# Performance work log

Measured on AMD Instinct MI355X. Metric: run time of the kernel, lower is better.

The kernel has to match this reference:

```python
import jax, jax.numpy as jnp
import numpy as np

B, T_NEW, D_MODEL, H, DH = 8, 512, 1024, 16, 64
CACHED = 2048
T_TOTAL = CACHED + T_NEW  # static padded total length (last batch item is full)


def setup_inputs() -> dict:
    key = jax.random.key(0)
    ks = jax.random.split(key, 16)
    x_new = jax.random.normal(ks[0], (B, T_NEW, D_MODEL), jnp.float32)
    past_lengths = jax.random.randint(ks[1], (B,), CACHED // 2, CACHED)
    past_lengths = past_lengths.at[-1].set(CACHED).astype(jnp.int32)
    new_counts = jax.random.randint(ks[2], (B,), 1, T_NEW)
    new_counts = new_counts.at[-1].set(T_NEW).astype(jnp.int32)
    # prefix (left-aligned) valid mask for new tokens, matching how the torch
    # module compacts k_new[b, :, :count] into the cache
    valid_new_mask = jnp.arange(T_NEW)[None, :] < new_counts[:, None]
    total_lengths = past_lengths + new_counts
    key_padding_mask = jnp.arange(T_TOTAL)[None, :] < total_lengths[:, None]
    inv_freq = 1.0 / (10000.0 ** (jnp.arange(0, DH, 2, dtype=jnp.float32) / DH))
    pm = (jnp.arange(CACHED)[None, :] < past_lengths[:, None])[:, None, :, None]
    past_k = jax.random.normal(ks[3], (B, H, CACHED, DH), jnp.float32) * pm
    past_v = jax.random.normal(ks[4], (B, H, CACHED, DH), jnp.float32) * pm
    s = 0.02
    Wq = jax.random.normal(ks[5], (D_MODEL, D_MODEL), jnp.float32) * s
    Wk = jax.random.normal(ks[6], (D_MODEL, D_MODEL), jnp.float32) * s
    Wv = jax.random.normal(ks[7], (D_MODEL, D_MODEL), jnp.float32) * s
    Wo = jax.random.normal(ks[8], (D_MODEL, D_MODEL), jnp.float32) * s
    bq = jnp.zeros((D_MODEL,), jnp.float32)
    bk = jnp.zeros((D_MODEL,), jnp.float32)
    bv = jnp.zeros((D_MODEL,), jnp.float32)
    bo = jnp.zeros((D_MODEL,), jnp.float32)
    return {
        'x_new': x_new, 'inv_freq': inv_freq, 'past_k': past_k, 'past_v': past_v,
        'Wq': Wq, 'bq': bq, 'Wk': Wk, 'bk': bk, 'Wv': Wv, 'bv': bv, 'Wo': Wo, 'bo': bo,
        'key_padding_mask': key_padding_mask, 'past_lengths': past_lengths,
        'valid_new_mask': valid_new_mask,
    }


def _rotate_half(x):
    h = x.shape[-1] // 2
    return jnp.concatenate([-x[..., h:], x[..., :h]], axis=-1)


def reference(x_new, inv_freq, past_k, past_v, Wq, bq, Wk, bk, Wv, bv, Wo, bo,
              key_padding_mask, past_lengths, valid_new_mask):
    Bb, Tn, _ = x_new.shape
    # projections -> [B, H, T_new, DH]
    q = (x_new @ Wq.T + bq).reshape(Bb, Tn, H, DH).transpose(0, 2, 1, 3)
    k_new = (x_new @ Wk.T + bk).reshape(Bb, Tn, H, DH).transpose(0, 2, 1, 3)
    v_new = (x_new @ Wv.T + bv).reshape(Bb, Tn, H, DH).transpose(0, 2, 1, 3)
    # RoPE at absolute positions past_len + step (invalid -> 0)
    steps = jnp.arange(Tn)
    positions = jnp.where(valid_new_mask, past_lengths[:, None] + steps[None, :], 0)
    freqs = positions[..., None].astype(jnp.float32) * inv_freq  # [B, T, DH/2]
    emb = jnp.concatenate([freqs, freqs], axis=-1)
    cos = jnp.cos(emb)[:, None].astype(q.dtype)  # [B, 1, T, DH]
    sin = jnp.sin(emb)[:, None].astype(q.dtype)
    q = q * cos + _rotate_half(q) * sin
    k_new = k_new * cos + _rotate_half(k_new) * sin
    vm = valid_new_mask[:, None, :, None].astype(q.dtype)
    q = q * vm
    k_new = k_new * vm
    v_new = v_new * vm
    # zero cached entries past each item's cached length (matches padded cache)
    pm = (jnp.arange(CACHED)[None, :] < past_lengths[:, None])[:, None, :, None]
    past_k = past_k * pm.astype(past_k.dtype)
    past_v = past_v * pm.astype(past_v.dtype)
    # ragged append: scatter new tokens at [past_len, past_len+count); invalid
    # tokens dumped into an extra slot T_TOTAL that is sliced off
    pos_idx = jnp.where(valid_new_mask, past_lengths[:, None] + steps[None, :], T_TOTAL)
    pad = lambda p: jnp.pad(p, ((0, 0), (0, 0), (0, T_TOTAL + 1 - CACHED), (0, 0)))
    scat = jax.vmap(lambda base, new, idx: base.at[:, idx, :].add(new))
    k_total = scat(pad(past_k), k_new, pos_idx)[:, :, :T_TOTAL]
    v_total = scat(pad(past_v), v_new, pos_idx)[:, :, :T_TOTAL]
    # padded SDPA with key-padding mask
    scores = jnp.einsum('bhqd,bhkd->bhqk', q, k_total) / jnp.sqrt(jnp.asarray(DH, q.dtype))
    scores = jnp.where(key_padding_mask[:, None, None, :], scores, jnp.finfo(scores.dtype).min)
    attn = jax.nn.softmax(scores, axis=-1)
    ctx = jnp.einsum('bhqk,bhkd->bhqd', attn, v_total)
    ctx = ctx.transpose(0, 2, 1, 3).reshape(Bb, Tn, D_MODEL)
    out = (ctx @ Wo.T + bo) * valid_new_mask[..., None].astype(ctx.dtype)
    total_lengths = past_lengths + valid_new_mask.sum(axis=1).astype(past_lengths.dtype)
    return out, k_total, v_total, total_lengths
```

## Files before the change

### kernel.cpp

```cpp
#include <hip/hip_runtime.h>
#include <math.h>

#define B_ 8
#define TN 512
#define DM 1024
#define H_ 16
#define DH 64
#define CACHED_ 2048
#define TT 2560

#define QSC 0.18033688011112042f

typedef __attribute__((ext_vector_type(8))) short bf16x8;
typedef __attribute__((ext_vector_type(4))) float f32x4;

union U16x8 { uint4 u; unsigned short s[8]; };
union U16x4 { uint2 u; unsigned short s[4]; };
union F4 { float4 v; float f[4]; };

__device__ __forceinline__ unsigned short f2b(float x) {
    unsigned u = __float_as_uint(x);
    unsigned r = (u + 0x7FFFu + ((u >> 16) & 1u)) >> 16;
    return (unsigned short)r;
}
__device__ __forceinline__ float b2f(unsigned short v) {
    return __uint_as_float((unsigned)v << 16);
}

__device__ __forceinline__ void gload16(const void* g, void* l) {
    __builtin_amdgcn_global_load_lds(
        (const __attribute__((address_space(1))) void*)g,
        (__attribute__((address_space(3))) void*)l, 16, 0, 0);
}

__global__ void count_kernel(const unsigned char* __restrict__ vnm,
                             const unsigned char* __restrict__ kpm,
                             const int* __restrict__ past_len,
                             int* __restrict__ counts,
                             float* __restrict__ total_out) {
    int b = blockIdx.x;
    __shared__ int red[256];
    int esz = (kpm[1] | kpm[2] | kpm[3]) ? 1 : 4;
    int s = 0;
    for (int t = threadIdx.x; t < TN; t += 256)
        s += (vnm[(size_t)(b * TN + t) * esz] != 0) ? 1 : 0;
    red[threadIdx.x] = s;
    __syncthreads();
    for (int off = 128; off > 0; off >>= 1) {
        if (threadIdx.x < off) red[threadIdx.x] += red[threadIdx.x + off];
        __syncthreads();
    }
    if (threadIdx.x == 0) {
        counts[b] = red[0];
        total_out[b] = (float)(past_len[b] + red[0]);
    }
}

__global__ void cvt_all(const float* __restrict__ x,
                        const float* __restrict__ Wq,
                        const float* __restrict__ Wk,
                        const float* __restrict__ Wv,
                        const float* __restrict__ Wo,
                        unsigned short* __restrict__ Xbf,
                        unsigned short* __restrict__ Wqkvb,
                        unsigned short* __restrict__ Wob) {
    int i8 = (blockIdx.x * 256 + threadIdx.x) << 3;
    const float* src;
    unsigned short* dst;
    int off;
    if (i8 < (1 << 22)) {
        src = x; off = i8; dst = Xbf + i8;
    } else if (i8 < (1 << 22) + (3 << 20)) {
        int j = i8 - (1 << 22);
        int w = j >> 20;
        src = w == 0 ? Wq : (w == 1 ? Wk : Wv);
        off = j & 0xFFFFF;
        dst = Wqkvb + j;
    } else {
        int j = i8 - ((1 << 22) + (3 << 20));
        src = Wo; off = j; dst = Wob + j;
    }
    float4 a = *(const float4*)(src + off);
    float4 b = *(const float4*)(src + off + 4);
    U16x8 o;
    o.s[0] = f2b(a.x); o.s[1] = f2b(a.y); o.s[2] = f2b(a.z); o.s[3] = f2b(a.w);
    o.s[4] = f2b(b.x); o.s[5] = f2b(b.y); o.s[6] = f2b(b.z); o.s[7] = f2b(b.w);
    *(uint4*)dst = o.u;
}

__device__ __forceinline__ void gemm_core(
    const unsigned short* __restrict__ A, const unsigned short* __restrict__ Bw,
    int K, int m0, int n0, short* As, short* Bs, f32x4 acc[4][4]) {
    const int tid = threadIdx.x;
    const int wave = tid >> 6, lane = tid & 63;
    const int wm = wave >> 1, wn = wave & 1;
    const int l15 = lane & 15, lq = lane >> 4;

    const int srow = wave * 16 + (lane >> 2);
    const int sc = (lane & 3) << 3;
    const unsigned short* Ag0 = A + (size_t)(m0 + srow) * K + sc;
    const unsigned short* Ag1 = A + (size_t)(m0 + 64 + srow) * K + sc;
    const unsigned short* Bg0 = Bw + (size_t)(n0 + srow) * K + sc;
    const unsigned short* Bg1 = Bw + (size_t)(n0 + 64 + srow) * K + sc;
    short* Ad0 = As + wave * 16 * 32;
    short* Ad1 = As + (64 + wave * 16) * 32;
    short* Bd0 = Bs + wave * 16 * 32;
    short* Bd1 = Bs + (64 + wave * 16) * 32;

    for (int k0 = 0; k0 < K; k0 += 32) {
        __syncthreads();
        gload16(Ag0 + k0, Ad0);
        gload16(Ag1 + k0, Ad1);
        gload16(Bg0 + k0, Bd0);
        gload16(Bg1 + k0, Bd1);
        __syncthreads();
        bf16x8 af[4], bf[4];
#pragma unroll
        for (int mi = 0; mi < 4; ++mi)
            af[mi] = *(const bf16x8*)&As[(wm * 64 + mi * 16 + l15) * 32 + lq * 8];
#pragma unroll
        for (int ni = 0; ni < 4; ++ni)
            bf[ni] = *(const bf16x8*)&Bs[(wn * 64 + ni * 16 + l15) * 32 + lq * 8];
#pragma unroll
        for (int mi = 0; mi < 4; ++mi)
#pragma unroll
            for (int ni = 0; ni < 4; ++ni)
                acc[mi][ni] = __builtin_amdgcn_mfma_f32_16x16x32_bf16(
                    af[mi], bf[ni], acc[mi][ni], 0, 0, 0);
    }
}

__global__ __launch_bounds__(256) void gemm_qkv_mfma(
    const unsigned short* __restrict__ Xbf,
    const unsigned short* __restrict__ Wqkv,
    const float* __restrict__ bq, const float* __restrict__ bk,
    const float* __restrict__ bv, const float* __restrict__ inv_freq,
    const int* __restrict__ past_len,
    unsigned short* __restrict__ Qraw, unsigned short* __restrict__ Kraw,
    unsigned short* __restrict__ Vraw) {
    __shared__ __align__(16) short As[128 * 32];
    __shared__ __align__(16) short Bs[128 * 32];
    f32x4 acc[4][4] = {};
    const int m0 = blockIdx.y << 7, n0 = blockIdx.x << 7;
    gemm_core(Xbf, Wqkv, DM, m0, n0, As, Bs, acc);

    const int which = n0 >> 10;
    const int tid = threadIdx.x, wave = tid >> 6, lane = tid & 63;
    const int wm = wave >> 1, wn = wave & 1, l15 = lane & 15, lq = lane >> 4;

    if (which == 0) {
        const int bb = m0 >> 9;
        const int pl = past_len[bb];
        const int hh = (n0 + wn * 64) >> 6;
#pragma unroll
        for (int ni = 0; ni < 2; ++ni) {
            int i = ni * 16 + l15;
            int n1 = n0 + wn * 64 + ni * 16 + l15;
            float fi = inv_freq[i];
            float blo = bq[n1], bhi = bq[n1 + 32];
#pragma unroll
            for (int mi = 0; mi < 4; ++mi) {
#pragma unroll
                for (int r = 0; r < 4; ++r) {
                    int m = m0 + wm * 64 + mi * 16 + lq * 4 + r;
                    int t = m & 511;
                    float ang = (float)(pl + t) * fi;
                    float s, c;
                    sincosf(ang, &s, &c);
                    float x1 = acc[mi][ni][r] + blo;
                    float x2 = acc[mi][ni + 2][r] + bhi;
                    size_t base = ((size_t)(bb * H_ + hh) * TN + t) * DH;
                    Qraw[base + i]      = f2b((x1 * c - x2 * s) * QSC);
                    Qraw[base + i + 32] = f2b((x2 * c + x1 * s) * QSC);
                }
            }
        }
    } else {
        const float* bias = which == 1 ? bk : bv;
        unsigned short* dst = which == 1 ? Kraw : Vraw;
#pragma unroll
        for (int ni = 0; ni < 4; ++ni) {
            int n1 = (n0 & 1023) + wn * 64 + ni * 16 + l15;
            float bb = bias[n1];
            int h = n1 >> 6, dh = n1 & 63;
#pragma unroll
            for (int mi = 0; mi < 4; ++mi) {
#pragma unroll
                for (int r = 0; r < 4; ++r) {
                    int m = m0 + wm * 64 + mi * 16 + lq * 4 + r;
                    int b = m >> 9, t = m & 511;
                    dst[((size_t)(b * H_ + h) * TN + t) * DH + dh] =
                        f2b(acc[mi][ni][r] + bb);
                }
            }
        }
    }
}

__global__ __launch_bounds__(256) void gemm_out_mfma(
    const unsigned short* __restrict__ Ctxb,
    const unsigned short* __restrict__ Wob,
    const float* __restrict__ bo, const int* __restrict__ counts,
    float* __restrict__ Out) {
    __shared__ __align__(16) short As[128 * 32];
    __shared__ __align__(16) short Bs[128 * 32];
    f32x4 acc[4][4] = {};
    const int m0 = blockIdx.y << 7, n0 = blockIdx.x << 7;
    gemm_core(Ctxb, Wob, DM, m0, n0, As, Bs, acc);

    const int tid = threadIdx.x, wave = tid >> 6, lane = tid & 63;
    const int wm = wave >> 1, wn = wave & 1, l15 = lane & 15, lq = lane >> 4;
    const int cnt = counts[m0 >> 9];
#pragma unroll
    for (int mi = 0; mi < 4; ++mi) {
#pragma unroll
        for (int r = 0; r < 4; ++r) {
            int m = m0 + wm * 64 + mi * 16 + lq * 4 + r;
            int t = m & 511;
            bool valid = t < cnt;
#pragma unroll
            for (int ni = 0; ni < 4; ++ni) {
                int n = n0 + wn * 64 + ni * 16 + l15;
                Out[(size_t)m * DM + n] = valid ? acc[mi][ni][r] + bo[n] : 0.f;
            }
        }
    }
}

__global__ void build_kv(const float* __restrict__ past_k,
                         const float* __restrict__ past_v,
                         const unsigned short* __restrict__ Kraw,
                         const unsigned short* __restrict__ Vraw,
                         const float* __restrict__ inv_freq,
                         const int* __restrict__ past_len,
                         const int* __restrict__ counts,
                         float* __restrict__ Ko, float* __restrict__ Vo,
                         unsigned short* __restrict__ Kb16,
                         unsigned short* __restrict__ Vb16) {
    int idx = blockIdx.x * 256 + threadIdx.x;
    int i = idx & 7;
    int p = idx >> 3;
    int h = blockIdx.y, bz = blockIdx.z;
    int pl = past_len[bz], cnt = counts[bz];
    int dh = i << 2;
    size_t obase = ((size_t)(bz * H_ + h) * TT + p) * DH;
    F4 k1, k2, v1, v2;
    if (p < pl) {
        size_t ib = ((size_t)(bz * H_ + h) * CACHED_ + p) * DH;
        k1.v = *(const float4*)(past_k + ib + dh);
        k2.v = *(const float4*)(past_k + ib + dh + 32);
        v1.v = *(const float4*)(past_v + ib + dh);
        v2.v = *(const float4*)(past_v + ib + dh + 32);
    } else if (p < pl + cnt) {
        int t = p - pl;
        size_t ib = ((size_t)(bz * H_ + h) * TN + t) * DH;
        U16x4 ka, kc, va, vc;
        ka.u = *(const uint2*)(Kraw + ib + dh);
        kc.u = *(const uint2*)(Kraw + ib + dh + 32);
        va.u = *(const uint2*)(Vraw + ib + dh);
        vc.u = *(const uint2*)(Vraw + ib + dh + 32);
#pragma unroll
        for (int j = 0; j < 4; ++j) {
            float ang = (float)p * inv_freq[dh + j];
            float s, c;
            sincosf(ang, &s, &c);
            float x1 = b2f(ka.s[j]), x2 = b2f(kc.s[j]);
            k1.f[j] = x1 * c - x2 * s;
            k2.f[j] = x2 * c + x1 * s;
            v1.f[j] = b2f(va.s[j]);
            v2.f[j] = b2f(vc.s[j]);
        }
    } else {
        k1.v = k2.v = v1.v = v2.v = make_float4(0.f, 0.f, 0.f, 0.f);
    }
    *(float4*)(Ko + obase + dh) = k1.v;
    *(float4*)(Ko + obase + dh + 32) = k2.v;
    *(float4*)(Vo + obase + dh) = v1.v;
    *(float4*)(Vo + obase + dh + 32) = v2.v;
    U16x4 o;
#pragma unroll
    for (int j = 0; j < 4; ++j) o.s[j] = f2b(k1.f[j]);
    *(uint2*)(Kb16 + obase + dh) = o.u;
#pragma unroll
    for (int j = 0; j < 4; ++j) o.s[j] = f2b(k2.f[j]);
    *(uint2*)(Kb16 + obase + dh + 32) = o.u;
#pragma unroll
    for (int j = 0; j < 4; ++j) o.s[j] = f2b(v1.f[j]);
    *(uint2*)(Vb16 + obase + dh) = o.u;
#pragma unroll
    for (int j = 0; j < 4; ++j) o.s[j] = f2b(v2.f[j]);
    *(uint2*)(Vb16 + obase + dh + 32) = o.u;
}

__global__ __launch_bounds__(256) void attn_mfma(
    const unsigned short* __restrict__ Qbf,
    const unsigned short* __restrict__ Kb,
    const unsigned short* __restrict__ Vb,
    const int* __restrict__ past_len, const int* __restrict__ counts,
    unsigned short* __restrict__ Ctxb) {
    const int qt = blockIdx.x, h = blockIdx.y, b = blockIdx.z;
    const int tid = threadIdx.x;
    const int wave = tid >> 6, lane = tid & 63;
    const int l15 = lane & 15, lq = lane >> 4;

    __shared__ __align__(16) short Qs[4096];
    __shared__ __align__(16) short Ks[4096];
    __shared__ __align__(16) short Vt[4096];
    __shared__ __align__(16) short Pb[4096];

    const size_t qbase = ((size_t)(b * H_ + h) * TN + qt * 64) * DH;
    const size_t kbase = (size_t)(b * H_ + h) * TT * DH;

    const int total = past_len[b] + counts[b];
    const int ntiles = (total + 63) >> 6;

    const int kp = tid & 31, dh8 = (tid >> 5) << 3;
    const int kc = kp >> 2, ko2 = (kp & 3) << 1;
    const unsigned short* Vg = Vb + kbase + (size_t)(2 * kp) * DH + dh8;
    uint4 vr0 = *(const uint4*)Vg;
    uint4 vr1 = *(const uint4*)(Vg + DH);

#pragma unroll
    for (int j = 0; j < 2; ++j) {
        int e = tid + (j << 8);
        int row = e >> 3, c = e & 7;
        *(uint4*)&Qs[(((row >> 4) * 8 + c) * 16 + ((row & 15) ^ c)) * 8] =
            *(const uint4*)(Qbf + qbase + row * 64 + c * 8);
    }
    __syncthreads();
    const int c0 = lq, c1 = 4 + lq;
    bf16x8 qa0 = *(const bf16x8*)&Qs[((wave * 8 + c0) * 16 + (l15 ^ c0)) * 8];
    bf16x8 qa1 = *(const bf16x8*)&Qs[((wave * 8 + c1) * 16 + (l15 ^ c1)) * 8];

    const int dA = wave * 64 + lane;
    const int dB = 256 + wave * 64 + lane;
    const int krA = (dA >> 7) * 16 + ((dA & 15) ^ ((dA >> 4) & 7));
    const int kcA = ((dA >> 4) & 7) << 3;
    const int krB = (dB >> 7) * 16 + ((dB & 15) ^ ((dB >> 4) & 7));
    const int kcB = ((dB >> 4) & 7) << 3;
    const unsigned short* KgA = Kb + kbase + (size_t)krA * DH + kcA;
    const unsigned short* KgB = Kb + kbase + (size_t)krB * DH + kcB;
    short* KdA = Ks + (size_t)(wave * 64) * 8;
    short* KdB = Ks + (size_t)(256 + wave * 64) * 8;

    float rsum[4] = {0.f, 0.f, 0.f, 0.f};
    f32x4 O[4] = {};
    short* Pw = Pb + wave * 1024;
    const int pc0 = l15 >> 3, pwo = l15 & 7;

    for (int kt = 0; kt < ntiles; ++kt) {
        __syncthreads();
        {
            U16x8 a, cc;
            a.u = vr0;
            cc.u = vr1;
#pragma unroll
            for (int j = 0; j < 8; ++j) {
                int dh = dh8 + j;
                unsigned pk = (unsigned)a.s[j] | ((unsigned)cc.s[j] << 16);
                *(unsigned*)&Vt[((((dh >> 4) * 8 + kc) * 16) + ((dh & 15) ^ kc)) * 8 + ko2] = pk;
            }
        }
        gload16(KgA + (size_t)kt * 64 * DH, KdA);
        gload16(KgB + (size_t)kt * 64 * DH, KdB);
        __syncthreads();

        {
            int ktn = (kt + 1 < ntiles) ? kt + 1 : kt;
            vr0 = *(const uint4*)(Vg + (size_t)ktn * 64 * DH);
            vr1 = *(const uint4*)(Vg + (size_t)ktn * 64 * DH + DH);
        }

        f32x4 S[4];
#pragma unroll
        for (int nt = 0; nt < 4; ++nt) {
            f32x4 acc = {};
            bf16x8 kb0 = *(const bf16x8*)&Ks[((nt * 8 + c0) * 16 + (l15 ^ c0)) * 8];
            acc = __builtin_amdgcn_mfma_f32_16x16x32_bf16(qa0, kb0, acc, 0, 0, 0);
            bf16x8 kb1 = *(const bf16x8*)&Ks[((nt * 8 + c1) * 16 + (l15 ^ c1)) * 8];
            acc = __builtin_amdgcn_mfma_f32_16x16x32_bf16(qa1, kb1, acc, 0, 0, 0);
            S[nt] = acc;
        }

        int limit = total - (kt << 6);
        if (limit < 64) {
#pragma unroll
            for (int nt = 0; nt < 4; ++nt) {
                bool ok = nt * 16 + l15 < limit;
#pragma unroll
                for (int r = 0; r < 4; ++r) S[nt][r] = ok ? S[nt][r] : -1e30f;
            }
        }

#pragma unroll
        for (int nt = 0; nt < 4; ++nt) {
            const int pc = nt * 2 + pc0;
#pragma unroll
            for (int r = 0; r < 4; ++r) {
                float p = __builtin_amdgcn_exp2f(S[nt][r]);
                rsum[r] += p;
                int row = lq * 4 + r;
                Pw[(pc * 16 + (row ^ pc)) * 8 + pwo] = (short)f2b(p);
            }
        }
        asm volatile("s_waitcnt lgkmcnt(0)" ::: "memory");

        bf16x8 pa0 = *(const bf16x8*)&Pw[(c0 * 16 + (l15 ^ c0)) * 8];
        bf16x8 pa1 = *(const bf16x8*)&Pw[(c1 * 16 + (l15 ^ c1)) * 8];
#pragma unroll
        for (int nt = 0; nt < 4; ++nt) {
            bf16x8 vb0 = *(const bf16x8*)&Vt[((nt * 8 + c0) * 16 + (l15 ^ c0)) * 8];
            O[nt] = __builtin_amdgcn_mfma_f32_16x16x32_bf16(pa0, vb0, O[nt], 0, 0, 0);
            bf16x8 vb1 = *(const bf16x8*)&Vt[((nt * 8 + c1) * 16 + (l15 ^ c1)) * 8];
            O[nt] = __builtin_amdgcn_mfma_f32_16x16x32_bf16(pa1, vb1, O[nt], 0, 0, 0);
        }
    }

#pragma unroll
    for (int off = 1; off < 16; off <<= 1)
#pragma unroll
        for (int r = 0; r < 4; ++r) rsum[r] += __shfl_xor(rsum[r], off);

#pragma unroll
    for (int r = 0; r < 4; ++r) {
        float inv = 1.f / rsum[r];
        int t = qt * 64 + wave * 16 + lq * 4 + r;
        size_t mbase = ((size_t)(b * TN + t)) * DM + h * DH;
#pragma unroll
        for (int nt = 0; nt < 4; ++nt)
            Ctxb[mbase + nt * 16 + l15] = f2b(O[nt][r] * inv);
    }
}

extern "C" void kernel_launch(void* const* d_in, const int* in_sizes, int n_in,
                              void* d_out, int out_size, void* d_ws, size_t ws_size,
                              hipStream_t stream) {
    const float* x_new    = (const float*)d_in[0];
    const float* inv_freq = (const float*)d_in[1];
    const float* past_k   = (const float*)d_in[2];
    const float* past_v   = (const float*)d_in[3];
    const float* Wq = (const float*)d_in[4];
    const float* bq = (const float*)d_in[5];
    const float* Wk = (const float*)d_in[6];
    const float* bk = (const float*)d_in[7];
    const float* Wv = (const float*)d_in[8];
    const float* bv = (const float*)d_in[9];
    const float* Wo = (const float*)d_in[10];
    const float* bo = (const float*)d_in[11];
    const unsigned char* kpm = (const unsigned char*)d_in[12];
    const int* past_len      = (const int*)d_in[13];
    const unsigned char* vnm = (const unsigned char*)d_in[14];

    float* out      = (float*)d_out;
    float* k_total  = out + (size_t)B_ * TN * DM;
    float* v_total  = k_total + (size_t)B_ * H_ * TT * DH;
    float* total_out = v_total + (size_t)B_ * H_ * TT * DH;

    const size_t NQ = (size_t)B_ * TN * DM;
    const size_t NKV = (size_t)B_ * H_ * TT * DH;

    int* counts = (int*)d_ws;
    unsigned short* Xbf   = (unsigned short*)((char*)d_ws + 256);
    unsigned short* Wqkvb = Xbf + NQ;
    unsigned short* Wob   = Wqkvb + (size_t)3 * DM * DM;
    unsigned short* Qraw  = Wob + (size_t)DM * DM;
    unsigned short* Kraw  = Qraw + NQ;
    unsigned short* Vraw  = Kraw + NQ;
    unsigned short* Ctxb  = Vraw + NQ;
    unsigned short* Kb16  = Ctxb + NQ;
    unsigned short* Vb16  = Kb16 + NKV;

    count_kernel<<<B_, 256, 0, stream>>>(vnm, kpm, past_len, counts, total_out);
    cvt_all<<<4096, 256, 0, stream>>>(x_new, Wq, Wk, Wv, Wo, Xbf, Wqkvb, Wob);

    gemm_qkv_mfma<<<dim3(24, 32), 256, 0, stream>>>(
        Xbf, Wqkvb, bq, bk, bv, inv_freq, past_len, Qraw, Kraw, Vraw);
    build_kv<<<dim3((TT * 8) / 256, H_, B_), 256, 0, stream>>>(
        past_k, past_v, Kraw, Vraw, inv_freq, past_len, counts,
        k_total, v_total, Kb16, Vb16);
    attn_mfma<<<dim3(TN / 64, H_, B_), 256, 0, stream>>>(Qraw, Kb16, Vb16,
                                                         past_len, counts, Ctxb);
    gemm_out_mfma<<<dim3(8, 32), 256, 0, stream>>>(Ctxb, Wob, bo, counts, out);
}
```

Before: 548.4 us.

## Double-buffer K tiles in attention and remap blocks so each XCD shares a (b,h)

Each K tile is now prefetched into a second LDS buffer one iteration ahead, replacing the per-tile __syncthreads pair with an explicit vmcnt wait plus barrier, so the global K load overlaps the MFMA work. The grid becomes 1D, and the block index is decoded so all eight query tiles of a given (batch, head) land on the same XCD, which is meant to improve L2 reuse of that head's K/V. The cost is an extra 8KB of LDS per block, which may lower occupancy, and the synchronisation is hand-managed, so its correctness depends on the wait counts.

```diff
diff --git a/kernel.cpp b/kernel.cpp
--- a/kernel.cpp
+++ b/kernel.cpp
@@ -298,13 +298,19 @@
     const unsigned short* __restrict__ Vb,
     const int* __restrict__ past_len, const int* __restrict__ counts,
     unsigned short* __restrict__ Ctxb) {
-    const int qt = blockIdx.x, h = blockIdx.y, b = blockIdx.z;
+    const int j = blockIdx.x;
+    const int xcd = j & 7;
+    const int tloc = j >> 3;
+    const int qt = tloc & 7;
+    const int p = ((tloc >> 3) << 3) | xcd;
+    const int b = p >> 4, h = p & 15;
+
     const int tid = threadIdx.x;
     const int wave = tid >> 6, lane = tid & 63;
     const int l15 = lane & 15, lq = lane >> 4;
 
     __shared__ __align__(16) short Qs[4096];
-    __shared__ __align__(16) short Ks[4096];
+    __shared__ __align__(16) short Ks[2][4096];
     __shared__ __align__(16) short Vt[4096];
     __shared__ __align__(16) short Pb[4096];
 
@@ -313,24 +319,6 @@
 
     const int total = past_len[b] + counts[b];
     const int ntiles = (total + 63) >> 6;
-
-    const int kp = tid & 31, dh8 = (tid >> 5) << 3;
-    const int kc = kp >> 2, ko2 = (kp & 3) << 1;
-    const unsigned short* Vg = Vb + kbase + (size_t)(2 * kp) * DH + dh8;
-    uint4 vr0 = *(const uint4*)Vg;
-    uint4 vr1 = *(const uint4*)(Vg + DH);
-
-#pragma unroll
-    for (int j = 0; j < 2; ++j) {
-        int e = tid + (j << 8);
-        int row = e >> 3, c = e & 7;
-        *(uint4*)&Qs[(((row >> 4) * 8 + c) * 16 + ((row & 15) ^ c)) * 8] =
-            *(const uint4*)(Qbf + qbase + row * 64 + c * 8);
-    }
-    __syncthreads();
-    const int c0 = lq, c1 = 4 + lq;
-    bf16x8 qa0 = *(const bf16x8*)&Qs[((wave * 8 + c0) * 16 + (l15 ^ c0)) * 8];
-    bf16x8 qa1 = *(const bf16x8*)&Qs[((wave * 8 + c1) * 16 + (l15 ^ c1)) * 8];
 
     const int dA = wave * 64 + lane;
     const int dB = 256 + wave * 64 + lane;
@@ -340,44 +328,71 @@
     const int kcB = ((dB >> 4) & 7) << 3;
     const unsigned short* KgA = Kb + kbase + (size_t)krA * DH + kcA;
     const unsigned short* KgB = Kb + kbase + (size_t)krB * DH + kcB;
-    short* KdA = Ks + (size_t)(wave * 64) * 8;
-    short* KdB = Ks + (size_t)(256 + wave * 64) * 8;
+    const int kdoffA = (wave * 64) * 8;
+    const int kdoffB = (256 + wave * 64) * 8;
+
+    gload16(KgA, &Ks[0][kdoffA]);
+    gload16(KgB, &Ks[0][kdoffB]);
+
+    const int kp = tid & 31, dh8 = (tid >> 5) << 3;
+    const int kc = kp >> 2, ko2 = (kp & 3) << 1;
+    const unsigned short* Vg = Vb + kbase + (size_t)(2 * kp) * DH + dh8;
+    uint4 vr0 = *(const uint4*)Vg;
+    uint4 vr1 = *(const uint4*)(Vg + DH);
+
+#pragma unroll
+    for (int jj = 0; jj < 2; ++jj) {
+        int e = tid + (jj << 8);
+        int row = e >> 3, c = e & 7;
+        *(uint4*)&Qs[(((row >> 4) * 8 + c) * 16 + ((row & 15) ^ c)) * 8] =
+            *(const uint4*)(Qbf + qbase + row * 64 + c * 8);
+    }
+    __syncthreads();
+    const int c0 = lq, c1 = 4 + lq;
+    bf16x8 qa0 = *(const bf16x8*)&Qs[((wave * 8 + c0) * 16 + (l15 ^ c0)) * 8];
+    bf16x8 qa1 = *(const bf16x8*)&Qs[((wave * 8 + c1) * 16 + (l15 ^ c1)) * 8];
 
     float rsum[4] = {0.f, 0.f, 0.f, 0.f};
     f32x4 O[4] = {};
     short* Pw = Pb + wave * 1024;
     const int pc0 = l15 >> 3, pwo = l15 & 7;
 
+    int cur = 0;
     for (int kt = 0; kt < ntiles; ++kt) {
-        __syncthreads();
+        asm volatile("s_waitcnt vmcnt(0)" ::: "memory");
+        __builtin_amdgcn_s_barrier();
+
         {
             U16x8 a, cc;
             a.u = vr0;
             cc.u = vr1;
 #pragma unroll
-            for (int j = 0; j < 8; ++j) {
-                int dh = dh8 + j;
-                unsigned pk = (unsigned)a.s[j] | ((unsigned)cc.s[j] << 16);
+            for (int jj = 0; jj < 8; ++jj) {
+                int dh = dh8 + jj;
+                unsigned pk = (unsigned)a.s[jj] | ((unsigned)cc.s[jj] << 16);
                 *(unsigned*)&Vt[((((dh >> 4) * 8 + kc) * 16) + ((dh & 15) ^ kc)) * 8 + ko2] = pk;
             }
         }
-        gload16(KgA + (size_t)kt * 64 * DH, KdA);
-        gload16(KgB + (size_t)kt * 64 * DH, KdB);
-        __syncthreads();
-
         {
             int ktn = (kt + 1 < ntiles) ? kt + 1 : kt;
+            gload16(KgA + (size_t)ktn * 64 * DH, &Ks[cur ^ 1][kdoffA]);
+            gload16(KgB + (size_t)ktn * 64 * DH, &Ks[cur ^ 1][kdoffB]);
             vr0 = *(const uint4*)(Vg + (size_t)ktn * 64 * DH);
             vr1 = *(const uint4*)(Vg + (size_t)ktn * 64 * DH + DH);
         }
 
+        asm volatile("s_waitcnt lgkmcnt(0)" ::: "memory");
+        __builtin_amdgcn_s_barrier();
+        __builtin_amdgcn_sched_barrier(0);
+
+        const short* Kcur = Ks[cur];
         f32x4 S[4];
 #pragma unroll
         for (int nt = 0; nt < 4; ++nt) {
             f32x4 acc = {};
-            bf16x8 kb0 = *(const bf16x8*)&Ks[((nt * 8 + c0) * 16 + (l15 ^ c0)) * 8];
+            bf16x8 kb0 = *(const bf16x8*)&Kcur[((nt * 8 + c0) * 16 + (l15 ^ c0)) * 8];
             acc = __builtin_amdgcn_mfma_f32_16x16x32_bf16(qa0, kb0, acc, 0, 0, 0);
-            bf16x8 kb1 = *(const bf16x8*)&Ks[((nt * 8 + c1) * 16 + (l15 ^ c1)) * 8];
+            bf16x8 kb1 = *(const bf16x8*)&Kcur[((nt * 8 + c1) * 16 + (l15 ^ c1)) * 8];
             acc = __builtin_amdgcn_mfma_f32_16x16x32_bf16(qa1, kb1, acc, 0, 0, 0);
             S[nt] = acc;
         }
@@ -397,10 +412,10 @@
             const int pc = nt * 2 + pc0;
 #pragma unroll
             for (int r = 0; r < 4; ++r) {
-                float p = __builtin_amdgcn_exp2f(S[nt][r]);
-                rsum[r] += p;
+                float pv = __builtin_amdgcn_exp2f(S[nt][r]);
+                rsum[r] += pv;
                 int row = lq * 4 + r;
-                Pw[(pc * 16 + (row ^ pc)) * 8 + pwo] = (short)f2b(p);
+                Pw[(pc * 16 + (row ^ pc)) * 8 + pwo] = (short)f2b(pv);
             }
         }
         asm volatile("s_waitcnt lgkmcnt(0)" ::: "memory");
@@ -414,6 +429,7 @@
             bf16x8 vb1 = *(const bf16x8*)&Vt[((nt * 8 + c1) * 16 + (l15 ^ c1)) * 8];
             O[nt] = __builtin_amdgcn_mfma_f32_16x16x32_bf16(pa1, vb1, O[nt], 0, 0, 0);
         }
+        cur ^= 1;
     }
 
 #pragma unroll
@@ -478,7 +494,7 @@
     build_kv<<<dim3((TT * 8) / 256, H_, B_), 256, 0, stream>>>(
         past_k, past_v, Kraw, Vraw, inv_freq, past_len, counts,
         k_total, v_total, Kb16, Vb16);
-    attn_mfma<<<dim3(TN / 64, H_, B_), 256, 0, stream>>>(Qraw, Kb16, Vb16,
-                                                         past_len, counts, Ctxb);
+    attn_mfma<<<1024, 256, 0, stream>>>(Qraw, Kb16, Vb16,
+                                        past_len, counts, Ctxb);
     gemm_out_mfma<<<dim3(8, 32), 256, 0, stream>>>(Ctxb, Wob, bo, counts, out);
 }
```

After: 532.8 us. -2.8%, faster.
